# Kernel tuning notes

Hardware: AMD Instinct MI355X
Metric: run time of the kernel (lower is better)

The kernel has to match this reference:

```python
import jax, jax.numpy as jnp
import numpy as np

NUM_HEADS = 12
HEAD_DIM = 64
ROPE_THETA = 10000.0
WINDOW = 128  # local_attention: total window, +/- WINDOW//2 around each query
NEG_INF = jnp.finfo(jnp.float32).min


def _rotate_half(x):
    x1, x2 = jnp.split(x, 2, axis=-1)
    return jnp.concatenate([-x2, x1], axis=-1)


def _rope_cos_sin(position_ids, head_dim, theta):
    # position_ids: [B, S] int -> cos/sin: [B, S, head_dim]
    inv_freq = 1.0 / (theta ** (jnp.arange(0, head_dim, 2, dtype=jnp.float32) / head_dim))
    freqs = position_ids.astype(jnp.float32)[..., None] * inv_freq  # [B, S, hd/2]
    emb = jnp.concatenate([freqs, freqs], axis=-1)  # [B, S, hd]
    return jnp.cos(emb), jnp.sin(emb)


def setup_inputs() -> dict:
    key = jax.random.key(0)
    k1, k2, k3 = jax.random.split(key, 3)
    B, S, H = 4, 2048, 768
    hidden_states = jax.random.normal(k1, (B, S, H), dtype=jnp.float32)
    position_ids = jnp.broadcast_to(jnp.arange(S, dtype=jnp.int64), (B, S))
    Wqkv = jax.random.normal(k2, (3 * H, H), dtype=jnp.float32) * 0.02
    Wo = jax.random.normal(k3, (H, H), dtype=jnp.float32) * 0.02
    return {"hidden_states": hidden_states, "position_ids": position_ids, "Wqkv": Wqkv, "Wo": Wo}


def reference(hidden_states, position_ids, Wqkv, Wo):
    B, S, H = hidden_states.shape
    nh, hd = NUM_HEADS, HEAD_DIM
    # QKV projection (no bias, attention_bias=False)
    qkv = jnp.einsum("bsh,oh->bso", hidden_states, Wqkv)  # [B, S, 3H]
    qkv = qkv.reshape(B, S, 3, nh, hd)
    # torch: qkv.transpose(3,1).unbind(dim=2) -> q,k,v: [B, nh, S, hd]
    qkv = jnp.transpose(qkv, (0, 3, 2, 1, 4))
    query, key, value = qkv[:, :, 0], qkv[:, :, 1], qkv[:, :, 2]
    # RoPE (NeoX style, non-interleaved)
    cos, sin = _rope_cos_sin(position_ids, hd, ROPE_THETA)  # [B, S, hd]
    cos = cos[:, None]  # [B, 1, S, hd]
    sin = sin[:, None]
    query = query * cos + _rotate_half(query) * sin
    key = key * cos + _rotate_half(key) * sin
    # sliding-window additive mask: attend iff |i - j| <= WINDOW // 2
    idx = jnp.arange(S)
    in_window = jnp.abs(idx[:, None] - idx[None, :]) <= (WINDOW // 2)
    mask = jnp.where(in_window, 0.0, NEG_INF)[None, None]  # [1, 1, S, S]
    scale = hd ** (-0.5)
    scores = jnp.einsum("bhqd,bhkd->bhqk", query, key) * scale + mask
    attn = jax.nn.softmax(scores.astype(jnp.float32), axis=-1).astype(query.dtype)
    out = jnp.einsum("bhqk,bhkd->bhqd", attn, value)  # [B, nh, S, hd]
    out = jnp.transpose(out, (0, 2, 1, 3)).reshape(B, S, H)
    # output projection
    return jnp.einsum("bsh,oh->bso", out, Wo)
```

## Files before the change

kernel.cpp:

```cpp
#include <hip/hip_runtime.h>
#include <hip/hip_bf16.h>

#define Bn 4
#define Sn 2048
#define Hn 768
#define NHn 12
#define Mn (Bn*Sn)
#define QKVN 2304

typedef unsigned short u16;
typedef unsigned int u32;
typedef __attribute__((ext_vector_type(8))) short short8;
typedef __attribute__((ext_vector_type(4))) float f32x4;

typedef __attribute__((address_space(1))) const u32 g_u32;
typedef __attribute__((address_space(3))) u32 l_u32;

__device__ __forceinline__ void gll16(const void* g, void* l) {
    __builtin_amdgcn_global_load_lds((g_u32*)g, (l_u32*)l, 16, 0, 0);
}

__device__ __forceinline__ u16 f2bf(float f) {
    u32 x = __float_as_uint(f);
    x += 0x7fffu + ((x >> 16) & 1u);
    return (u16)(x >> 16);
}
__device__ __forceinline__ float bf2f(u16 u) {
    return __uint_as_float(((u32)u) << 16);
}

#define KWAIT(N) do { \
    asm volatile("s_waitcnt vmcnt(" #N ")" ::: "memory"); \
    __builtin_amdgcn_s_barrier(); \
    __builtin_amdgcn_sched_barrier(0); \
} while (0)

__global__ __launch_bounds__(256) void prep_k(const float* __restrict__ hs,
                                              const float* __restrict__ wqkv,
                                              const float* __restrict__ wo,
                                              const int* __restrict__ pos_ids,
                                              u16* __restrict__ hs_b,
                                              u16* __restrict__ wqkv_b,
                                              u16* __restrict__ wo_b,
                                              float2* __restrict__ tab) {
    int i = blockIdx.x * 256 + threadIdx.x;
    if (i < 262144) {
        int d2 = i & 31, row = i >> 5;
        float invf = exp2f((float)d2 * -0.4152410119f);
        float fr = (float)pos_ids[row] * invf;
        float sn, cs;
        sincosf(fr, &sn, &cs);
        tab[i] = make_float2(cs, sn);
        return;
    }
    i -= 262144;
    const float* s; u16* d; int off;
    if (i < 1572864)      { s = hs;   d = hs_b;   off = i; }
    else if (i < 2015232) { s = wqkv; d = wqkv_b; off = i - 1572864; }
    else if (i < 2162688) { s = wo;   d = wo_b;   off = i - 2015232; }
    else return;
    float4 v = ((const float4*)s)[off];
    ushort4 o;
    o.x = f2bf(v.x); o.y = f2bf(v.y); o.z = f2bf(v.z); o.w = f2bf(v.w);
    ((ushort4*)d)[off] = o;
}

template <typename OUT, bool ROPE>
__global__ __launch_bounds__(256, 3) void gemm_pl(const u16* __restrict__ A,
                                                  const u16* __restrict__ Bw,
                                                  OUT* __restrict__ C,
                                                  const float2* __restrict__ tab,
                                                  int N, int K) {
    __shared__ __align__(16) u16 As[3][128 * 32];
    __shared__ __align__(16) u16 Bs[3][128 * 32];
    const int t = threadIdx.x;
    const int wid = t >> 6, lane = t & 63;
    const int wr = wid >> 1, wc = wid & 1;
    const long m0 = (long)blockIdx.x * 128;
    const long n0 = (long)blockIdx.y * 128;
    const int lr = lane & 15, g = lane >> 4;

    f32x4 acc[4][4] = {};

    auto stage = [&](int slot, int kt) {
        #pragma unroll
        for (int j = 0; j < 2; ++j) {
            int idx = t + j * 256;
            int row = idx >> 2, gg = idx & 3;
            int col8 = (gg ^ (row & 3)) * 8;
            gll16(A + (m0 + row) * K + kt * 32 + col8, (char*)As[slot] + idx * 16);
        }
        #pragma unroll
        for (int j = 0; j < 2; ++j) {
            int idx = t + j * 256;
            int row = idx >> 2, gg = idx & 3;
            int col8 = (gg ^ (row & 3)) * 8;
            gll16(Bw + (n0 + row) * K + kt * 32 + col8, (char*)Bs[slot] + idx * 16);
        }
    };

    auto compute = [&](int slot, int stslot, int kt) {
        if (kt >= 0) stage(stslot, kt);
        const u16* Ab = As[slot];
        const u16* Bb = Bs[slot];
        short8 af[4], bfr[4];
        #pragma unroll
        for (int nt = 0; nt < 4; ++nt) {
            int row = wc * 64 + nt * 16 + lr;
            bfr[nt] = *(const short8*)((const char*)Bb + row * 64 +
                                       ((g ^ (row & 3)) << 4));
        }
        #pragma unroll
        for (int mt = 0; mt < 4; ++mt) {
            int row = wr * 64 + mt * 16 + lr;
            af[mt] = *(const short8*)((const char*)Ab + row * 64 +
                                      ((g ^ (row & 3)) << 4));
        }
        __builtin_amdgcn_s_setprio(1);
        #pragma unroll
        for (int mt = 0; mt < 4; ++mt)
            #pragma unroll
            for (int nt = 0; nt < 4; ++nt)
                acc[mt][nt] = __builtin_amdgcn_mfma_f32_16x16x32_bf16(
                    af[mt], bfr[nt], acc[mt][nt], 0, 0, 0);
        __builtin_amdgcn_s_setprio(0);
    };

    const int NT = K / 32;
    stage(0, 0);
    stage(1, 1);
    int sl = 0;
    for (int it = 0; it + 2 < NT; ++it) {
        KWAIT(4);
        int s2 = sl + 2; if (s2 >= 3) s2 -= 3;
        compute(sl, s2, it + 2);
        ++sl; if (sl == 3) sl = 0;
    }
    KWAIT(4); compute(sl, 0, -1);
    ++sl; if (sl == 3) sl = 0;
    KWAIT(0); compute(sl, 0, -1);

    if constexpr (ROPE) {
        if ((n0 + wc * 64) < 1536) {
            #pragma unroll
            for (int mt = 0; mt < 4; ++mt)
                #pragma unroll
                for (int r = 0; r < 4; ++r) {
                    long row = m0 + wr * 64 + mt * 16 + g * 4 + r;
                    const float2* tr = tab + row * 32;
                    #pragma unroll
                    for (int ntp = 0; ntp < 2; ++ntp) {
                        float2 cssn = tr[ntp * 16 + lr];
                        float x1 = acc[mt][ntp][r], x2 = acc[mt][ntp + 2][r];
                        acc[mt][ntp][r]     = x1 * cssn.x - x2 * cssn.y;
                        acc[mt][ntp + 2][r] = x2 * cssn.x + x1 * cssn.y;
                    }
                }
        }
    }

    #pragma unroll
    for (int mt = 0; mt < 4; ++mt)
        #pragma unroll
        for (int nt = 0; nt < 4; ++nt)
            #pragma unroll
            for (int r = 0; r < 4; ++r) {
                long row = m0 + wr * 64 + mt * 16 + g * 4 + r;
                long col = n0 + wc * 64 + nt * 16 + lr;
                float v = acc[mt][nt][r];
                if constexpr (sizeof(OUT) == 2) C[row * N + col] = (OUT)f2bf(v);
                else                            C[row * N + col] = v;
            }
}

__global__ __launch_bounds__(256) void attn_k(const u16* __restrict__ qkv,
                                              u16* __restrict__ outb) {
    const int qt = blockIdx.x, bh = blockIdx.y;
    const int b = bh / NHn, h = bh % NHn;
    const int q0 = qt * 64, kv0 = q0 - 64;
    const int t = threadIdx.x, wid = t >> 6, lane = t & 63;
    const int lr = lane & 15, g = lane >> 4;

    __shared__ __align__(16) char smem[58368];
    u16* Qs = (u16*)smem;
    u16* Ks = (u16*)(smem + 8192);
    u16* Vt = (u16*)(smem + 32768);

    const size_t rowbase = (size_t)b * Sn;

    #pragma unroll
    for (int ss = 0; ss < 2; ++ss) {
        int s = t + ss * 256;
        int row = s >> 3, gg = s & 7;
        int col8 = (gg ^ (row & 7)) * 8;
        gll16(qkv + (rowbase + q0 + row) * QKVN + h * 64 + col8, (char*)Qs + s * 16);
    }
    #pragma unroll
    for (int ss = 0; ss < 6; ++ss) {
        int s = t + ss * 256;
        int row = s >> 3, gg = s & 7;
        int kk = kv0 + row;
        kk = kk < 0 ? 0 : (kk > Sn - 1 ? Sn - 1 : kk);
        int col8 = (gg ^ (row & 7)) * 8;
        gll16(qkv + (rowbase + kk) * QKVN + 768 + h * 64 + col8, (char*)Ks + s * 16);
    }
    #pragma unroll
    for (int ss = 0; ss < 6; ++ss) {
        int s = t + ss * 256;
        int krow = s >> 3, gg = s & 7;
        int kk = kv0 + krow;
        kk = kk < 0 ? 0 : (kk > Sn - 1 ? Sn - 1 : kk);
        short8 v = *(const short8*)(qkv + (rowbase + kk) * QKVN + 1536 + h * 64 + gg * 8);
        #pragma unroll
        for (int j = 0; j < 8; ++j) Vt[(gg * 8 + j) * 200 + krow] = (u16)v[j];
    }
    __syncthreads();

    f32x4 sacc[12] = {};
    #pragma unroll
    for (int kk2 = 0; kk2 < 2; ++kk2) {
        int qrow = wid * 16 + lr;
        int slot = kk2 * 4 + g;
        short8 qf = *(const short8*)((const char*)Qs + qrow * 128 + ((slot ^ (qrow & 7)) << 4));
        #pragma unroll
        for (int tl = 0; tl < 12; ++tl) {
            int krow = tl * 16 + lr;
            short8 kf = *(const short8*)((const char*)Ks + krow * 128 + ((slot ^ (krow & 7)) << 4));
            sacc[tl] = __builtin_amdgcn_mfma_f32_16x16x32_bf16(qf, kf, sacc[tl], 0, 0, 0);
        }
    }

    float p[12][4];
    float lsum[4];
    #pragma unroll
    for (int r = 0; r < 4; ++r) {
        int qq = q0 + wid * 16 + g * 4 + r;
        float mx = -3.0e38f;
        #pragma unroll
        for (int tl = 0; tl < 12; ++tl) {
            int kq = kv0 + tl * 16 + lr;
            float sc = sacc[tl][r] * 0.125f;
            int dqk = qq - kq;
            bool valid = (kq >= 0) && (kq < Sn) && (dqk <= 64) && (dqk >= -64);
            sc = valid ? sc : -3.0e38f;
            p[tl][r] = sc;
            mx = fmaxf(mx, sc);
        }
        #pragma unroll
        for (int mk = 1; mk < 16; mk <<= 1) mx = fmaxf(mx, __shfl_xor(mx, mk, 16));
        float sum = 0.f;
        #pragma unroll
        for (int tl = 0; tl < 12; ++tl) {
            float e = __expf(p[tl][r] - mx);
            p[tl][r] = e;
            sum += e;
        }
        #pragma unroll
        for (int mk = 1; mk < 16; mk <<= 1) sum += __shfl_xor(sum, mk, 16);
        lsum[r] = sum;
    }

    __syncthreads();

    u16* Pw = (u16*)(smem + wid * 6400);
    #pragma unroll
    for (int tl = 0; tl < 12; ++tl)
        #pragma unroll
        for (int r = 0; r < 4; ++r)
            Pw[(g * 4 + r) * 200 + tl * 16 + lr] = f2bf(p[tl][r]);

    f32x4 oacc[4] = {};
    #pragma unroll
    for (int ks = 0; ks < 6; ++ks) {
        short8 pf = *(const short8*)((const char*)Pw + lr * 400 + (ks * 32 + g * 8) * 2);
        #pragma unroll
        for (int dt = 0; dt < 4; ++dt) {
            short8 vf = *(const short8*)((const char*)Vt + (dt * 16 + lr) * 400 + (ks * 32 + g * 8) * 2);
            oacc[dt] = __builtin_amdgcn_mfma_f32_16x16x32_bf16(pf, vf, oacc[dt], 0, 0, 0);
        }
    }

    #pragma unroll
    for (int dt = 0; dt < 4; ++dt)
        #pragma unroll
        for (int r = 0; r < 4; ++r) {
            int row = q0 + wid * 16 + g * 4 + r;
            float v = oacc[dt][r] / lsum[r];
            outb[(rowbase + row) * Hn + h * 64 + dt * 16 + lr] = f2bf(v);
        }
}

extern "C" void kernel_launch(void* const* d_in, const int* in_sizes, int n_in,
                              void* d_out, int out_size, void* d_ws, size_t ws_size,
                              hipStream_t stream) {
    const float* hs   = (const float*)d_in[0];
    const int*   pos  = (const int*)d_in[1];
    const float* wqkv = (const float*)d_in[2];
    const float* wo   = (const float*)d_in[3];
    float* out = (float*)d_out;
    char* ws = (char*)d_ws;

    u16* hs_b   = (u16*)(ws);
    u16* wqkv_b = (u16*)(ws + 12582912);
    u16* wo_b   = (u16*)(ws + 16121856);
    u16* qkv    = (u16*)(ws + 17301504);
    u16* attn   = (u16*)(ws + 55050240);
    float2* tab = (float2*)(ws + 55050240);

    prep_k<<<9472, 256, 0, stream>>>(hs, wqkv, wo, pos, hs_b, wqkv_b, wo_b, tab);

    gemm_pl<u16, true><<<dim3(64, 18), 256, 0, stream>>>(
        hs_b, wqkv_b, qkv, tab, 2304, 768);

    attn_k<<<dim3(32, 48), 256, 0, stream>>>(qkv, attn);

    gemm_pl<float, false><<<dim3(64, 6), 256, 0, stream>>>(
        attn, wo_b, out, nullptr, 768, 768);
}
```

Baseline: 108.3 us.

## Switch GEMM to BK=64 double-buffered pipeline with in-slot refill after barrier

The GEMM pipeline moves from three 32-wide K slots to two 64-wide slots. Each compute step first reads both k-halves of its fragments into registers, waits on LDS, and barriers. It then refills the same slot with the stage two steps ahead and runs 32 MFMAs per step. This halves the number of iteration and wait overheads and gives more MFMA work per sync, but it uses more LDS (64KB vs 48KB), lowers the occupancy target to 2, and adds a barrier per step.

Result: faster. 100.6 us (-7.2%).

```diff
diff --git a/kernel.cpp b/kernel.cpp
--- a/kernel.cpp
+++ b/kernel.cpp
@@ -66,13 +66,13 @@
 }
 
 template <typename OUT, bool ROPE>
-__global__ __launch_bounds__(256, 3) void gemm_pl(const u16* __restrict__ A,
+__global__ __launch_bounds__(256, 2) void gemm_p2(const u16* __restrict__ A,
                                                   const u16* __restrict__ Bw,
                                                   OUT* __restrict__ C,
                                                   const float2* __restrict__ tab,
                                                   int N, int K) {
-    __shared__ __align__(16) u16 As[3][128 * 32];
-    __shared__ __align__(16) u16 Bs[3][128 * 32];
+    __shared__ __align__(16) u16 As[2][128 * 64];
+    __shared__ __align__(16) u16 Bs[2][128 * 64];
     const int t = threadIdx.x;
     const int wid = t >> 6, lane = t & 63;
     const int wr = wid >> 1, wc = wid & 1;
@@ -84,61 +84,66 @@
 
     auto stage = [&](int slot, int kt) {
         #pragma unroll
-        for (int j = 0; j < 2; ++j) {
+        for (int j = 0; j < 4; ++j) {
             int idx = t + j * 256;
-            int row = idx >> 2, gg = idx & 3;
-            int col8 = (gg ^ (row & 3)) * 8;
-            gll16(A + (m0 + row) * K + kt * 32 + col8, (char*)As[slot] + idx * 16);
-        }
-        #pragma unroll
-        for (int j = 0; j < 2; ++j) {
+            int row = idx >> 3, gg = idx & 7;
+            int col8 = (gg ^ (row & 7)) * 8;
+            gll16(A + (m0 + row) * K + kt * 64 + col8, (char*)As[slot] + idx * 16);
+        }
+        #pragma unroll
+        for (int j = 0; j < 4; ++j) {
             int idx = t + j * 256;
-            int row = idx >> 2, gg = idx & 3;
-            int col8 = (gg ^ (row & 3)) * 8;
-            gll16(Bw + (n0 + row) * K + kt * 32 + col8, (char*)Bs[slot] + idx * 16);
+            int row = idx >> 3, gg = idx & 7;
+            int col8 = (gg ^ (row & 7)) * 8;
+            gll16(Bw + (n0 + row) * K + kt * 64 + col8, (char*)Bs[slot] + idx * 16);
         }
     };
 
-    auto compute = [&](int slot, int stslot, int kt) {
-        if (kt >= 0) stage(stslot, kt);
+    auto compute = [&](int slot, int kstage) {
         const u16* Ab = As[slot];
         const u16* Bb = Bs[slot];
-        short8 af[4], bfr[4];
-        #pragma unroll
-        for (int nt = 0; nt < 4; ++nt) {
-            int row = wc * 64 + nt * 16 + lr;
-            bfr[nt] = *(const short8*)((const char*)Bb + row * 64 +
-                                       ((g ^ (row & 3)) << 4));
-        }
-        #pragma unroll
-        for (int mt = 0; mt < 4; ++mt) {
-            int row = wr * 64 + mt * 16 + lr;
-            af[mt] = *(const short8*)((const char*)Ab + row * 64 +
-                                      ((g ^ (row & 3)) << 4));
-        }
+        short8 af[2][4], bfr[2][4];
+        #pragma unroll
+        for (int kk2 = 0; kk2 < 2; ++kk2) {
+            const int gs = kk2 * 4 + g;
+            #pragma unroll
+            for (int nt = 0; nt < 4; ++nt) {
+                int row = wc * 64 + nt * 16 + lr;
+                bfr[kk2][nt] = *(const short8*)((const char*)Bb + row * 128 +
+                                                ((gs ^ (row & 7)) << 4));
+            }
+            #pragma unroll
+            for (int mt = 0; mt < 4; ++mt) {
+                int row = wr * 64 + mt * 16 + lr;
+                af[kk2][mt] = *(const short8*)((const char*)Ab + row * 128 +
+                                               ((gs ^ (row & 7)) << 4));
+            }
+        }
+        asm volatile("s_waitcnt lgkmcnt(0)" ::: "memory");
+        __builtin_amdgcn_s_barrier();
+        __builtin_amdgcn_sched_barrier(0);
+        if (kstage >= 0) stage(slot, kstage);
         __builtin_amdgcn_s_setprio(1);
         #pragma unroll
-        for (int mt = 0; mt < 4; ++mt)
-            #pragma unroll
-            for (int nt = 0; nt < 4; ++nt)
-                acc[mt][nt] = __builtin_amdgcn_mfma_f32_16x16x32_bf16(
-                    af[mt], bfr[nt], acc[mt][nt], 0, 0, 0);
+        for (int kk2 = 0; kk2 < 2; ++kk2)
+            #pragma unroll
+            for (int mt = 0; mt < 4; ++mt)
+                #pragma unroll
+                for (int nt = 0; nt < 4; ++nt)
+                    acc[mt][nt] = __builtin_amdgcn_mfma_f32_16x16x32_bf16(
+                        af[kk2][mt], bfr[kk2][nt], acc[mt][nt], 0, 0, 0);
         __builtin_amdgcn_s_setprio(0);
     };
 
-    const int NT = K / 32;
+    const int NT = K / 64;
     stage(0, 0);
     stage(1, 1);
-    int sl = 0;
     for (int it = 0; it + 2 < NT; ++it) {
-        KWAIT(4);
-        int s2 = sl + 2; if (s2 >= 3) s2 -= 3;
-        compute(sl, s2, it + 2);
-        ++sl; if (sl == 3) sl = 0;
-    }
-    KWAIT(4); compute(sl, 0, -1);
-    ++sl; if (sl == 3) sl = 0;
-    KWAIT(0); compute(sl, 0, -1);
+        KWAIT(8);
+        compute(it & 1, it + 2);
+    }
+    KWAIT(8); compute(NT & 1, -1);
+    KWAIT(0); compute((NT - 1) & 1, -1);
 
     if constexpr (ROPE) {
         if ((n0 + wc * 64) < 1536) {
@@ -309,11 +314,11 @@
 
     prep_k<<<9472, 256, 0, stream>>>(hs, wqkv, wo, pos, hs_b, wqkv_b, wo_b, tab);
 
-    gemm_pl<u16, true><<<dim3(64, 18), 256, 0, stream>>>(
+    gemm_p2<u16, true><<<dim3(64, 18), 256, 0, stream>>>(
         hs_b, wqkv_b, qkv, tab, 2304, 768);
 
     attn_k<<<dim3(32, 48), 256, 0, stream>>>(qkv, attn);
 
-    gemm_pl<float, false><<<dim3(64, 6), 256, 0, stream>>>(
+    gemm_p2<float, false><<<dim3(64, 6), 256, 0, stream>>>(
         attn, wo_b, out, nullptr, 768, 768);
 }
```

## Deepen GEMM pipeline to four LDS stages with XCD-aware block swizzle

Applied to the files above, without the earlier changes.

The bf16 GEMM kernel goes from a 3-slot to a 4-slot LDS ring with three tiles in flight. The next tile's async load is now issued after the current fragments are read from LDS. The LDS XOR swizzle changes to use (row>>1)&3 to reduce bank conflicts on 16-byte fragment reads. A 1D grid is remapped so consecutive blocks on each XCD share A/B tiles for better L2 reuse. Launch bounds drop to 2 blocks per CU to fit the larger LDS footprint, which costs occupancy.

Result: slower. 121.6 us (+12.2%).

```diff
diff --git a/kernel.cpp b/kernel.cpp
--- a/kernel.cpp
+++ b/kernel.cpp
@@ -66,19 +66,23 @@
 }
 
 template <typename OUT, bool ROPE>
-__global__ __launch_bounds__(256, 3) void gemm_pl(const u16* __restrict__ A,
+__global__ __launch_bounds__(256, 2) void gemm_p4(const u16* __restrict__ A,
                                                   const u16* __restrict__ Bw,
                                                   OUT* __restrict__ C,
                                                   const float2* __restrict__ tab,
-                                                  int N, int K) {
-    __shared__ __align__(16) u16 As[3][128 * 32];
-    __shared__ __align__(16) u16 Bs[3][128 * 32];
+                                                  int N, int K, int nbx) {
+    __shared__ __align__(16) u16 As[4][128 * 32];
+    __shared__ __align__(16) u16 Bs[4][128 * 32];
     const int t = threadIdx.x;
     const int wid = t >> 6, lane = t & 63;
     const int wr = wid >> 1, wc = wid & 1;
-    const long m0 = (long)blockIdx.x * 128;
-    const long n0 = (long)blockIdx.y * 128;
     const int lr = lane & 15, g = lane >> 4;
+
+    const int nb = gridDim.x;
+    const int bid = blockIdx.x;
+    const int sw = (bid & 7) * (nb >> 3) + (bid >> 3);
+    const long m0 = (long)(sw % nbx) * 128;
+    const long n0 = (long)(sw / nbx) * 128;
 
     f32x4 acc[4][4] = {};
 
@@ -87,20 +91,19 @@
         for (int j = 0; j < 2; ++j) {
             int idx = t + j * 256;
             int row = idx >> 2, gg = idx & 3;
-            int col8 = (gg ^ (row & 3)) * 8;
+            int col8 = (gg ^ ((row >> 1) & 3)) * 8;
             gll16(A + (m0 + row) * K + kt * 32 + col8, (char*)As[slot] + idx * 16);
         }
         #pragma unroll
         for (int j = 0; j < 2; ++j) {
             int idx = t + j * 256;
             int row = idx >> 2, gg = idx & 3;
-            int col8 = (gg ^ (row & 3)) * 8;
+            int col8 = (gg ^ ((row >> 1) & 3)) * 8;
             gll16(Bw + (n0 + row) * K + kt * 32 + col8, (char*)Bs[slot] + idx * 16);
         }
     };
 
-    auto compute = [&](int slot, int stslot, int kt) {
-        if (kt >= 0) stage(stslot, kt);
+    auto compute = [&](int slot, int kstage) {
         const u16* Ab = As[slot];
         const u16* Bb = Bs[slot];
         short8 af[4], bfr[4];
@@ -108,14 +111,15 @@
         for (int nt = 0; nt < 4; ++nt) {
             int row = wc * 64 + nt * 16 + lr;
             bfr[nt] = *(const short8*)((const char*)Bb + row * 64 +
-                                       ((g ^ (row & 3)) << 4));
+                                       ((g ^ ((row >> 1) & 3)) << 4));
         }
         #pragma unroll
         for (int mt = 0; mt < 4; ++mt) {
             int row = wr * 64 + mt * 16 + lr;
             af[mt] = *(const short8*)((const char*)Ab + row * 64 +
-                                      ((g ^ (row & 3)) << 4));
-        }
+                                      ((g ^ ((row >> 1) & 3)) << 4));
+        }
+        if (kstage >= 0) stage(kstage & 3, kstage);
         __builtin_amdgcn_s_setprio(1);
         #pragma unroll
         for (int mt = 0; mt < 4; ++mt)
@@ -129,16 +133,14 @@
     const int NT = K / 32;
     stage(0, 0);
     stage(1, 1);
-    int sl = 0;
-    for (int it = 0; it + 2 < NT; ++it) {
-        KWAIT(4);
-        int s2 = sl + 2; if (s2 >= 3) s2 -= 3;
-        compute(sl, s2, it + 2);
-        ++sl; if (sl == 3) sl = 0;
-    }
-    KWAIT(4); compute(sl, 0, -1);
-    ++sl; if (sl == 3) sl = 0;
-    KWAIT(0); compute(sl, 0, -1);
+    stage(2, 2);
+    for (int it = 0; it + 3 < NT; ++it) {
+        KWAIT(8);
+        compute(it & 3, it + 3);
+    }
+    KWAIT(8); compute((NT - 3) & 3, -1);
+    KWAIT(4); compute((NT - 2) & 3, -1);
+    KWAIT(0); compute((NT - 1) & 3, -1);
 
     if constexpr (ROPE) {
         if ((n0 + wc * 64) < 1536) {
@@ -309,11 +311,11 @@
 
     prep_k<<<9472, 256, 0, stream>>>(hs, wqkv, wo, pos, hs_b, wqkv_b, wo_b, tab);
 
-    gemm_pl<u16, true><<<dim3(64, 18), 256, 0, stream>>>(
-        hs_b, wqkv_b, qkv, tab, 2304, 768);
+    gemm_p4<u16, true><<<1152, 256, 0, stream>>>(
+        hs_b, wqkv_b, qkv, tab, 2304, 768, 64);
 
     attn_k<<<dim3(32, 48), 256, 0, stream>>>(qkv, attn);
 
-    gemm_pl<float, false><<<dim3(64, 6), 256, 0, stream>>>(
-        attn, wo_b, out, nullptr, 768, 768);
-}
+    gemm_p4<float, false><<<384, 256, 0, stream>>>(
+        attn, wo_b, out, nullptr, 768, 768, 64);
+}
```
